# Kernel tuning notes

Hardware: AMD Instinct MI355X
Metric: run time of the kernel (lower is better)

Reference implementation:

```python
import jax, jax.numpy as jnp
import numpy as np

N = 131072
C = 8
W = 256


def setup_inputs() -> dict:
    key = jax.random.key(0)
    ks = jax.random.split(key, 10)
    s1 = 1.0 / np.sqrt(3.0)
    sw = 1.0 / np.sqrt(W)
    return {
        "positions": jax.random.normal(ks[0], (N, 3), dtype=jnp.float32),
        "times": jax.random.randint(ks[1], (N,), 0, C, dtype=jnp.int64),
        "W1": jax.random.normal(ks[2], (C, 3, W), dtype=jnp.float32) * s1,
        "b1": jnp.zeros((C, W), dtype=jnp.float32),
        "W2": jax.random.normal(ks[3], (C, W, W), dtype=jnp.float32) * sw,
        "b2": jnp.zeros((C, W), dtype=jnp.float32),
        "W3": jax.random.normal(ks[4], (C, W, W), dtype=jnp.float32) * sw,
        "b3": jnp.zeros((C, W), dtype=jnp.float32),
        "W4": jax.random.normal(ks[5], (C, W, 3), dtype=jnp.float32) * sw,
        "b4": jnp.zeros((C, 3), dtype=jnp.float32),
    }


def _mlp(x, w1, c1, w2, c2, w3, c3, w4, c4):
    # 4-layer MLP, Tanh hidden activations and Tanh output activation
    h = jnp.tanh(x @ w1 + c1)
    h = jnp.tanh(h @ w2 + c2)
    h = jnp.tanh(h @ w3 + c3)
    return jnp.tanh(h @ w4 + c4)


def reference(positions, times, W1, b1, W2, b2, W3, b3, W4, b4):
    # offsets = zeros_like(positions); offsets[times==i] = mlp_i(positions[times==i])
    # classes partition the points, so this equals a per-class select-sum.
    offsets = jnp.zeros_like(positions)
    for i in range(C):  # small fixed class count
        out_i = _mlp(positions, W1[i], b1[i], W2[i], b2[i], W3[i], b3[i], W4[i], b4[i])
        mask = (times == i)[:, None]  # [N,1]
        offsets = jnp.where(mask, out_i, offsets)
    return offsets
```

## Files before the change

kernel.cpp:

```cpp
#include <hip/hip_runtime.h>
#include <stdint.h>

#define N_PTS 131072
#define NCLS 8
#define HID 256
#define MT 64
#define CAP 32768

typedef __bf16 bf16x8 __attribute__((ext_vector_type(8)));
typedef float f32x4 __attribute__((ext_vector_type(4)));

__device__ __forceinline__ float tanh_p2(float a) {
  return fmaf(-2.0f, __builtin_amdgcn_rcpf(__expf(a) + 1.0f), 1.0f);
}

__device__ __forceinline__ unsigned short f2bf_rne(float f) {
  unsigned u = __float_as_uint(f);
  u = u + 0x7fffu + ((u >> 16) & 1u);
  return (unsigned short)(u >> 16);
}

__device__ __forceinline__ unsigned pack_bf16(float a, float b) {
  unsigned ua = __float_as_uint(a) + 0x8000u;
  unsigned ub = __float_as_uint(b) + 0x8000u;
  return __builtin_amdgcn_perm(ub, ua, 0x07060302u);
}

#define PK_TILES 256
#define MISC_BLKS 177
#define MISC_N 45184
#define SCAT_BLKS 128
#define PREP_GRID (PK_TILES + MISC_BLKS + SCAT_BLKS)

__global__ __launch_bounds__(256) void k_prep(
    const int* __restrict__ times,
    const float* __restrict__ W1, const float* __restrict__ b1,
    const float* __restrict__ W2, const float* __restrict__ b2,
    const float* __restrict__ W3, const float* __restrict__ b3,
    const float* __restrict__ W4, const float* __restrict__ b4,
    int* __restrict__ hdr, int* __restrict__ sortedIdx,
    unsigned short* __restrict__ packed23,
    float* __restrict__ w1p, float* __restrict__ b2p,
    float* __restrict__ b3p, float* __restrict__ b4p,
    unsigned short* __restrict__ W4p) {
  __shared__ unsigned short T[64][64];

  int b = blockIdx.x;
  int tid = threadIdx.x;

  if (b < PK_TILES) {
    int cl = b >> 4;
    int l = cl >> 3, c = cl & 7;
    int tile = b & 15;
    int k0 = (tile >> 2) * 64, j0 = (tile & 3) * 64;
    const float* W = (l ? W3 : W2) + c * 65536;
#pragma unroll
    for (int it = 0; it < 4; it++) {
      int f = tid + it * 256;
      int row = f >> 4, cg = f & 15;
      float4 v = *(const float4*)&W[(k0 + row) * 256 + j0 + cg * 4];
      T[row][cg * 4 + 0] = f2bf_rne(2.0f * v.x);
      T[row][cg * 4 + 1] = f2bf_rne(2.0f * v.y);
      T[row][cg * 4 + 2] = f2bf_rne(2.0f * v.z);
      T[row][cg * 4 + 3] = f2bf_rne(2.0f * v.w);
    }
    __syncthreads();
#pragma unroll
    for (int it = 0; it < 2; it++) {
      int g = tid + it * 256;
      int kb = g >> 6, j = g & 63;
      unsigned u[8];
#pragma unroll
      for (int uu = 0; uu < 8; uu++) u[uu] = T[kb * 8 + uu][j];
      uint4 pk = make_uint4(u[0] | (u[1] << 16), u[2] | (u[3] << 16),
                            u[4] | (u[5] << 16), u[6] | (u[7] << 16));
      int base = cl * 65536 + (((k0 >> 3) + kb) * 256 + (j0 + j)) * 8;
      *(uint4*)&packed23[base] = pk;
    }
  } else if (b < PK_TILES + MISC_BLKS) {
    int e2 = (b - PK_TILES) * 256 + tid;
    if (e2 < 8192) {
      int c = e2 >> 10, rem = e2 & 1023;
      int j = rem >> 2, t = rem & 3;
      float v = (t < 3) ? W1[c * 768 + t * 256 + j] : b1[c * 256 + j];
      w1p[e2] = 2.0f * v;
    } else if (e2 < 10240) {
      int i = e2 - 8192;
      b2p[i] = 2.0f * b2[i];
    } else if (e2 < 12288) {
      int i = e2 - 10240;
      b3p[i] = 2.0f * b3[i];
    } else if (e2 < 12416) {
      int i = e2 - 12288;
      int c = i >> 4, r = i & 15;
      b4p[i] = (r < 3) ? 2.0f * b4[c * 3 + r] : 0.0f;
    } else if (e2 < MISC_N) {
      int i = e2 - 12416;
      int c = i >> 12, rem = i & 4095;
      int jj = rem & 7, j = (rem >> 3) & 15, k = ((rem >> 7) << 3) + jj;
      float v = (j < 3) ? 2.0f * W4[c * 768 + k * 3 + j] : 0.0f;
      W4p[c * 4096 + rem] = f2bf_rne(v);
    }
  } else {
    __shared__ int gcnt[16][NCLS];
    __shared__ int gpre[16][NCLS];
    __shared__ int gbase[NCLS];
    int sb = b - (PK_TILES + MISC_BLKS);
    int lane = tid & 63, w = tid >> 6;
    int4 tv = ((const int4*)times)[sb * 256 + tid];
    int tcl[4] = {tv.x, tv.y, tv.z, tv.w};
    int rank[4];
#pragma unroll
    for (int s = 0; s < 4; s++) {
      int t = tcl[s];
      unsigned long long m0 = __ballot(t == 0), m1 = __ballot(t == 1);
      unsigned long long m2 = __ballot(t == 2), m3 = __ballot(t == 3);
      unsigned long long m4 = __ballot(t == 4), m5 = __ballot(t == 5);
      unsigned long long m6 = __ballot(t == 6), m7 = __ballot(t == 7);
      unsigned long long x0 = (t & 1) ? m1 : m0, x1 = (t & 1) ? m3 : m2;
      unsigned long long x2 = (t & 1) ? m5 : m4, x3 = (t & 1) ? m7 : m6;
      unsigned long long y0 = (t & 2) ? x1 : x0, y1 = (t & 2) ? x3 : x2;
      unsigned long long mo = (t & 4) ? y1 : y0;
      rank[s] = __popcll(mo & ((1ull << lane) - 1ull));
      if (lane == 0) {
        int g = w * 4 + s;
        gcnt[g][0] = __popcll(m0); gcnt[g][1] = __popcll(m1);
        gcnt[g][2] = __popcll(m2); gcnt[g][3] = __popcll(m3);
        gcnt[g][4] = __popcll(m4); gcnt[g][5] = __popcll(m5);
        gcnt[g][6] = __popcll(m6); gcnt[g][7] = __popcll(m7);
      }
    }
    __syncthreads();
    if (tid < NCLS) {
      int run = 0;
#pragma unroll
      for (int g = 0; g < 16; g++) { gpre[g][tid] = run; run += gcnt[g][tid]; }
      gbase[tid] = run ? atomicAdd(&hdr[tid], run) : 0;
    }
    __syncthreads();
    int i0 = (sb * 256 + tid) * 4;
#pragma unroll
    for (int s = 0; s < 4; s++) {
      int t = tcl[s];
      int g = w * 4 + s;
      sortedIdx[t * CAP + gbase[t] + gpre[g][t] + rank[s]] = i0 + s;
    }
  }
}

__device__ __forceinline__ void mfma_layer_T(
    unsigned short (*__restrict__ Abuf)[MT][8],
    const unsigned short* __restrict__ Apack,
    const float* __restrict__ biasp,
    int tid) {
  int lane = tid & 63, w = tid >> 6;
  int quad = lane >> 4, l16 = lane & 15;
  int jcol = w * 32 + l16;
  const bf16x8* __restrict__ Af = (const bf16x8*)Apack;

  f32x4 acc[2][4];
#pragma unroll
  for (int jf = 0; jf < 2; jf++) {
    f32x4 bv = *(const f32x4*)&biasp[w * 32 + jf * 16 + quad * 4];
#pragma unroll
    for (int mt = 0; mt < 4; mt++) acc[jf][mt] = bv;
  }

#pragma unroll
  for (int kb = 0; kb < 8; kb++) {
    int kq = kb * 4 + quad;
    bf16x8 af[2], bfr[4];
#pragma unroll
    for (int jf = 0; jf < 2; jf++) af[jf] = Af[kq * 256 + jcol + jf * 16];
#pragma unroll
    for (int mt = 0; mt < 4; mt++)
      bfr[mt] = *(const bf16x8*)&Abuf[kq][mt * 16 + l16][0];
#pragma unroll
    for (int jf = 0; jf < 2; jf++)
#pragma unroll
      for (int mt = 0; mt < 4; mt++)
        acc[jf][mt] = __builtin_amdgcn_mfma_f32_16x16x32_bf16(af[jf], bfr[mt], acc[jf][mt], 0, 0, 0);
  }

  __syncthreads();

#pragma unroll
  for (int jf = 0; jf < 2; jf++) {
    int jbase = w * 32 + jf * 16 + quad * 4;
#pragma unroll
    for (int mt = 0; mt < 4; mt++) {
      float t0 = tanh_p2(acc[jf][mt][0]);
      float t1 = tanh_p2(acc[jf][mt][1]);
      float t2 = tanh_p2(acc[jf][mt][2]);
      float t3 = tanh_p2(acc[jf][mt][3]);
      uint2 pk = make_uint2(pack_bf16(t0, t1), pack_bf16(t2, t3));
      *(uint2*)&Abuf[jbase >> 3][mt * 16 + l16][jbase & 7] = pk;
    }
  }
}

__global__ __launch_bounds__(512, 6) void k_mlp(
    const float* __restrict__ pos,
    const int* __restrict__ hdr, const int* __restrict__ sortedIdx,
    const unsigned short* __restrict__ packed23,
    const float* __restrict__ w1p, const float* __restrict__ b2p,
    const float* __restrict__ b3p, const float* __restrict__ b4p,
    const unsigned short* __restrict__ W4p,
    float* __restrict__ out) {

  __shared__ __align__(16) unsigned short Abuf[32][MT][8];
  __shared__ __align__(16) float4 w1i[256];
  __shared__ __align__(16) float4 xpos4[MT];
  __shared__ int sIdx[MT];

  int b = blockIdx.x;
  int tid = threadIdx.x;

  int c = -1, t0 = 0, cnt = 0;
  {
    int ts = 0;
#pragma unroll
    for (int cc = 0; cc < NCLS; cc++) {
      int cc_cnt = hdr[cc];
      int tiles = (cc_cnt + MT - 1) >> 6;
      if (b >= ts && b < ts + tiles) { c = cc; t0 = b - ts; cnt = cc_cnt; }
      ts += tiles;
    }
  }
  if (c < 0) return;
  int base = c * CAP + t0 * MT;
  int mCount = min(MT, cnt - t0 * MT);

  if (tid < MT) sIdx[tid] = sortedIdx[base + min(tid, mCount - 1)];
  if (tid < 256) w1i[tid] = ((const float4*)(w1p + (size_t)c * 1024))[tid];
  __syncthreads();
  if (tid < MT) {
    int idx = sIdx[tid] * 3;
    xpos4[tid] = make_float4(pos[idx], pos[idx + 1], pos[idx + 2], 0.0f);
  }
  __syncthreads();

  {
    int m = tid & 63, q = tid >> 6;
    float4 xp = xpos4[m];
#pragma unroll
    for (int i8 = 0; i8 < 4; i8++) {
      int j8 = q * 4 + i8;
      unsigned pk[4];
#pragma unroll
      for (int jp = 0; jp < 4; jp++) {
        float t[2];
#pragma unroll
        for (int u = 0; u < 2; u++) {
          float4 wv = w1i[j8 * 8 + jp * 2 + u];
          float a = fmaf(xp.x, wv.x, fmaf(xp.y, wv.y, fmaf(xp.z, wv.z, wv.w)));
          t[u] = tanh_p2(a);
        }
        pk[jp] = pack_bf16(t[0], t[1]);
      }
      *(uint4*)&Abuf[j8][m][0] = make_uint4(pk[0], pk[1], pk[2], pk[3]);
    }
  }
  __syncthreads();

  mfma_layer_T(Abuf, packed23 + ((size_t)c << 16), b2p + c * 256, tid);
  __syncthreads();
  mfma_layer_T(Abuf, packed23 + ((size_t)(8 + c) << 16), b3p + c * 256, tid);
  __syncthreads();

  {
    int lane = tid & 63, w = tid >> 6;
    if (w < 4) {
      int quad = lane >> 4, l16 = lane & 15;
      f32x4 acc = *(const f32x4*)&b4p[c * 16 + quad * 4];
#pragma unroll
      for (int kb = 0; kb < 8; kb++) {
        int kq = kb * 4 + quad;
        bf16x8 a4 = *(const bf16x8*)&W4p[((size_t)c * 512 + kq * 16 + l16) * 8];
        bf16x8 b4f = *(const bf16x8*)&Abuf[kq][w * 16 + l16][0];
        acc = __builtin_amdgcn_mfma_f32_16x16x32_bf16(a4, b4f, acc, 0, 0, 0);
      }
      int m = w * 16 + l16;
      if (quad == 0 && m < mCount) {
        int o = sIdx[m] * 3;
        out[o + 0] = tanh_p2(acc[0]);
        out[o + 1] = tanh_p2(acc[1]);
        out[o + 2] = tanh_p2(acc[2]);
      }
    }
  }
}

extern "C" void kernel_launch(void* const* d_in, const int* in_sizes, int n_in,
                              void* d_out, int out_size, void* d_ws, size_t ws_size,
                              hipStream_t stream) {
  const float* pos = (const float*)d_in[0];
  const int* times = (const int*)d_in[1];
  const float* W1 = (const float*)d_in[2];
  const float* b1 = (const float*)d_in[3];
  const float* W2 = (const float*)d_in[4];
  const float* b2 = (const float*)d_in[5];
  const float* W3 = (const float*)d_in[6];
  const float* b3 = (const float*)d_in[7];
  const float* W4 = (const float*)d_in[8];
  const float* b4 = (const float*)d_in[9];

  char* ws = (char*)d_ws;
  int* hdr = (int*)ws;
  int* sortedIdx = (int*)(ws + 4096);
  float* w1p = (float*)(ws + 1052672);
  float* b2p = (float*)(ws + 1085440);
  float* b3p = (float*)(ws + 1093632);
  float* b4p = (float*)(ws + 1101824);
  unsigned short* W4p = (unsigned short*)(ws + 1102336);
  unsigned short* packed23 = (unsigned short*)(ws + (2u << 20));
  float* out = (float*)d_out;

  hipMemsetAsync(d_ws, 0, 64, stream);
  k_prep<<<PREP_GRID, 256, 0, stream>>>(times, W1, b1, W2, b2, W3, b3, W4, b4,
                                        hdr, sortedIdx, packed23,
                                        w1p, b2p, b3p, b4p, W4p);
  k_mlp<<<N_PTS / MT + NCLS, 512, 0, stream>>>(
      pos, hdr, sortedIdx, packed23, w1p, b2p, b3p, b4p, W4p, out);
}
```

Measured before the change: 128.7 us.

## Prefetch next layer's first weight fragments, fold log2e into weights, raise MFMA priority

Scales all weights and biases by 2*log2(e) instead of 2 during packing, so tanh can use a raw exp2 instruction rather than expf with its internal multiply. Each MFMA layer now uses weight fragments for its first k-block that were loaded during the previous stage, and issues the loads for the next layer's first fragments before the barrier and tanh epilogue. This is meant to hide global-load latency at layer boundaries. It also wraps the MFMA loops in s_setprio to favour the matrix-issuing waves, at the cost of extra registers held across stages.

```diff
diff --git a/kernel.cpp b/kernel.cpp
--- a/kernel.cpp
+++ b/kernel.cpp
@@ -7,11 +7,13 @@
 #define MT 64
 #define CAP 32768
 
+#define PSC 2.8853900817779268f
+
 typedef __bf16 bf16x8 __attribute__((ext_vector_type(8)));
 typedef float f32x4 __attribute__((ext_vector_type(4)));
 
 __device__ __forceinline__ float tanh_p2(float a) {
-  return fmaf(-2.0f, __builtin_amdgcn_rcpf(__expf(a) + 1.0f), 1.0f);
+  return fmaf(-2.0f, __builtin_amdgcn_rcpf(__builtin_amdgcn_exp2f(a) + 1.0f), 1.0f);
 }
 
 __device__ __forceinline__ unsigned short f2bf_rne(float f) {
@@ -59,10 +61,10 @@
       int f = tid + it * 256;
       int row = f >> 4, cg = f & 15;
       float4 v = *(const float4*)&W[(k0 + row) * 256 + j0 + cg * 4];
-      T[row][cg * 4 + 0] = f2bf_rne(2.0f * v.x);
-      T[row][cg * 4 + 1] = f2bf_rne(2.0f * v.y);
-      T[row][cg * 4 + 2] = f2bf_rne(2.0f * v.z);
-      T[row][cg * 4 + 3] = f2bf_rne(2.0f * v.w);
+      T[row][cg * 4 + 0] = f2bf_rne(PSC * v.x);
+      T[row][cg * 4 + 1] = f2bf_rne(PSC * v.y);
+      T[row][cg * 4 + 2] = f2bf_rne(PSC * v.z);
+      T[row][cg * 4 + 3] = f2bf_rne(PSC * v.w);
     }
     __syncthreads();
 #pragma unroll
@@ -83,22 +85,22 @@
       int c = e2 >> 10, rem = e2 & 1023;
       int j = rem >> 2, t = rem & 3;
       float v = (t < 3) ? W1[c * 768 + t * 256 + j] : b1[c * 256 + j];
-      w1p[e2] = 2.0f * v;
+      w1p[e2] = PSC * v;
     } else if (e2 < 10240) {
       int i = e2 - 8192;
-      b2p[i] = 2.0f * b2[i];
+      b2p[i] = PSC * b2[i];
     } else if (e2 < 12288) {
       int i = e2 - 10240;
-      b3p[i] = 2.0f * b3[i];
+      b3p[i] = PSC * b3[i];
     } else if (e2 < 12416) {
       int i = e2 - 12288;
       int c = i >> 4, r = i & 15;
-      b4p[i] = (r < 3) ? 2.0f * b4[c * 3 + r] : 0.0f;
+      b4p[i] = (r < 3) ? PSC * b4[c * 3 + r] : 0.0f;
     } else if (e2 < MISC_N) {
       int i = e2 - 12416;
       int c = i >> 12, rem = i & 4095;
       int jj = rem & 7, j = (rem >> 3) & 15, k = ((rem >> 7) << 3) + jj;
-      float v = (j < 3) ? 2.0f * W4[c * 768 + k * 3 + j] : 0.0f;
+      float v = (j < 3) ? PSC * W4[c * 768 + k * 3 + j] : 0.0f;
       W4p[c * 4096 + rem] = f2bf_rne(v);
     }
   } else {
@@ -148,11 +150,15 @@
   }
 }
 
+struct AfPre { bf16x8 a0, a1; };
+
 __device__ __forceinline__ void mfma_layer_T(
     unsigned short (*__restrict__ Abuf)[MT][8],
     const unsigned short* __restrict__ Apack,
     const float* __restrict__ biasp,
-    int tid) {
+    int tid, const AfPre& pre,
+    const bf16x8* __restrict__ np0, const bf16x8* __restrict__ np1,
+    AfPre& nxt) {
   int lane = tid & 63, w = tid >> 6;
   int quad = lane >> 4, l16 = lane & 15;
   int jcol = w * 32 + l16;
@@ -166,12 +172,17 @@
     for (int mt = 0; mt < 4; mt++) acc[jf][mt] = bv;
   }
 
+  __builtin_amdgcn_s_setprio(1);
 #pragma unroll
   for (int kb = 0; kb < 8; kb++) {
     int kq = kb * 4 + quad;
     bf16x8 af[2], bfr[4];
-#pragma unroll
-    for (int jf = 0; jf < 2; jf++) af[jf] = Af[kq * 256 + jcol + jf * 16];
+    if (kb == 0) {
+      af[0] = pre.a0; af[1] = pre.a1;
+    } else {
+#pragma unroll
+      for (int jf = 0; jf < 2; jf++) af[jf] = Af[kq * 256 + jcol + jf * 16];
+    }
 #pragma unroll
     for (int mt = 0; mt < 4; mt++)
       bfr[mt] = *(const bf16x8*)&Abuf[kq][mt * 16 + l16][0];
@@ -181,6 +192,10 @@
       for (int mt = 0; mt < 4; mt++)
         acc[jf][mt] = __builtin_amdgcn_mfma_f32_16x16x32_bf16(af[jf], bfr[mt], acc[jf][mt], 0, 0, 0);
   }
+  __builtin_amdgcn_s_setprio(0);
+
+  nxt.a0 = *np0;
+  nxt.a1 = *np1;
 
   __syncthreads();
 
@@ -231,6 +246,10 @@
   int base = c * CAP + t0 * MT;
   int mCount = min(MT, cnt - t0 * MT);
 
+  int lane = tid & 63, w = tid >> 6;
+  int quad = lane >> 4, l16 = lane & 15;
+  int jcol = w * 32 + l16;
+
   if (tid < MT) sIdx[tid] = sortedIdx[base + min(tid, mCount - 1)];
   if (tid < 256) w1i[tid] = ((const float4*)(w1p + (size_t)c * 1024))[tid];
   __syncthreads();
@@ -238,6 +257,13 @@
     int idx = sIdx[tid] * 3;
     xpos4[tid] = make_float4(pos[idx], pos[idx + 1], pos[idx + 2], 0.0f);
   }
+
+  const bf16x8* __restrict__ Af2 = (const bf16x8*)(packed23 + ((size_t)c << 16));
+  const bf16x8* __restrict__ Af3 = (const bf16x8*)(packed23 + ((size_t)(8 + c) << 16));
+  const bf16x8* __restrict__ W4f = (const bf16x8*)W4p;
+  AfPre pre2, pre3, pre4;
+  pre2.a0 = Af2[quad * 256 + jcol];
+  pre2.a1 = Af2[quad * 256 + jcol + 16];
   __syncthreads();
 
   {
@@ -263,23 +289,29 @@
   }
   __syncthreads();
 
-  mfma_layer_T(Abuf, packed23 + ((size_t)c << 16), b2p + c * 256, tid);
-  __syncthreads();
-  mfma_layer_T(Abuf, packed23 + ((size_t)(8 + c) << 16), b3p + c * 256, tid);
+  mfma_layer_T(Abuf, packed23 + ((size_t)c << 16), b2p + c * 256, tid, pre2,
+               &Af3[quad * 256 + jcol], &Af3[quad * 256 + jcol + 16], pre3);
+  __syncthreads();
+  mfma_layer_T(Abuf, packed23 + ((size_t)(8 + c) << 16), b3p + c * 256, tid, pre3,
+               &W4f[(size_t)c * 512 + quad * 16 + l16],
+               &W4f[(size_t)c * 512 + (quad + 4) * 16 + l16], pre4);
   __syncthreads();
 
   {
-    int lane = tid & 63, w = tid >> 6;
     if (w < 4) {
-      int quad = lane >> 4, l16 = lane & 15;
       f32x4 acc = *(const f32x4*)&b4p[c * 16 + quad * 4];
+      __builtin_amdgcn_s_setprio(1);
 #pragma unroll
       for (int kb = 0; kb < 8; kb++) {
         int kq = kb * 4 + quad;
-        bf16x8 a4 = *(const bf16x8*)&W4p[((size_t)c * 512 + kq * 16 + l16) * 8];
+        bf16x8 a4;
+        if (kb == 0) a4 = pre4.a0;
+        else if (kb == 1) a4 = pre4.a1;
+        else a4 = W4f[(size_t)c * 512 + kq * 16 + l16];
         bf16x8 b4f = *(const bf16x8*)&Abuf[kq][w * 16 + l16][0];
         acc = __builtin_amdgcn_mfma_f32_16x16x32_bf16(a4, b4f, acc, 0, 0, 0);
       }
+      __builtin_amdgcn_s_setprio(0);
       int m = w * 16 + l16;
       if (quad == 0 && m < mCount) {
         int o = sIdx[m] * 3;
```

Measured after the change: 128.6 us (median of 2 runs). Within noise of the previous version (-0.1%).
